# Performance work log

Hardware: AMD Instinct MI355X
Metric: run time of the kernel (lower is better)

The kernel has to match this reference:

```python
import jax, jax.numpy as jnp
import numpy as np
import math

L, H, E, D = 4, 8, 256, 32  # layers, heads, embed, head_dim
SCALE = 1.0 / math.sqrt(D)

def _ln(x, w, b, eps=1e-5):
    mu = jnp.mean(x, -1, keepdims=True)
    var = jnp.mean((x - mu) ** 2, -1, keepdims=True)
    return (x - mu) * jax.lax.rsqrt(var + eps) * w + b

def setup_inputs() -> dict:
    key = jax.random.key(0)
    ks = jax.random.split(key, 16)
    B, S, C = 32, 512, 512
    w = lambda k, sh: jax.random.normal(k, sh, jnp.float32) * 0.05
    return {
        'cnn_features': jax.random.normal(ks[0], (B, S, C), jnp.float32),
        'cnn_w': w(ks[1], (E, C)), 'cnn_b': jnp.zeros((E,), jnp.float32),
        'tok_emb': w(ks[2], (2, E)),
        'Wq': w(ks[3], (L, E, E)), 'bq': jnp.zeros((L, E), jnp.float32),
        'Wk': w(ks[4], (L, E, E)), 'bk': jnp.zeros((L, E), jnp.float32),
        'Wv': w(ks[5], (L, E, E)), 'bv': jnp.zeros((L, E), jnp.float32),
        'Wo': w(ks[6], (L, E, E)), 'bo': jnp.zeros((L, E), jnp.float32),
        'ln1_w': jnp.ones((L, E), jnp.float32), 'ln1_b': jnp.zeros((L, E), jnp.float32),
        'ln2_w': jnp.ones((L, E), jnp.float32), 'ln2_b': jnp.zeros((L, E), jnp.float32),
        'mlp_w1': w(ks[7], (L, 3 * E, E)), 'mlp_b1': jnp.zeros((L, 3 * E), jnp.float32),
        'mlp_w2': w(ks[8], (L, E, 3 * E)), 'mlp_b2': jnp.zeros((L, E), jnp.float32),
        'lnf_w': jnp.ones((E,), jnp.float32), 'lnf_b': jnp.zeros((E,), jnp.float32),
        'out_w1': w(ks[9], (2 * E, E)), 'out_b1': jnp.zeros((2 * E,), jnp.float32),
        'out_w2': w(ks[10], (C, 2 * E)), 'out_b2': jnp.zeros((C,), jnp.float32),
    }

def _forward(cnn_features, cnn_w, cnn_b, tok_emb, Wq, bq, Wk, bk, Wv, bv, Wo, bo,
             ln1_w, ln1_b, ln2_w, ln2_b, mlp_w1, mlp_b1, mlp_w2, mlp_b2,
             lnf_w, lnf_b, out_w1, out_b1, out_w2, out_b2):
    B, S, _ = cnn_features.shape
    # CNN feature projection + token-type embedding (all tokens type 0)
    x = cnn_features @ cnn_w.T + cnn_b + tok_emb[0]  # [B,S,E]
    for i in range(L):
        q = (x @ Wq[i].T + bq[i]).reshape(B, S, H, D).transpose(0, 2, 1, 3)
        k = (x @ Wk[i].T + bk[i]).reshape(B, S, H, D).transpose(0, 2, 1, 3)
        v = (x @ Wv[i].T + bv[i]).reshape(B, S, H, D).transpose(0, 2, 1, 3)
        scores = jnp.einsum('bhqd,bhkd->bhqk', q, k) * SCALE
        attn = jax.nn.softmax(scores, axis=-1)  # dropout = identity (eval)
        attended = jnp.einsum('bhqk,bhkd->bhqd', attn, v)
        attended = attended.transpose(0, 2, 1, 3).reshape(B, S, E)
        attn_out = attended @ Wo[i].T + bo[i]
        x = _ln(x + attn_out, ln1_w[i], ln1_b[i])
        h = jax.nn.gelu(x @ mlp_w1[i].T + mlp_b1[i], approximate=False)
        mlp_out = h @ mlp_w2[i].T + mlp_b2[i]
        x = _ln(x + mlp_out, ln2_w[i], ln2_b[i])
    x = _ln(x, lnf_w, lnf_b)
    h = jax.nn.gelu(x @ out_w1.T + out_b1, approximate=False)
    out = jax.nn.relu(h @ out_w2.T + out_b2)  # [B,S,cnn_feature_dim]
    return out

def reference(cnn_features, cnn_w, cnn_b, tok_emb, Wq, bq, Wk, bk, Wv, bv, Wo, bo,
              ln1_w, ln1_b, ln2_w, ln2_b, mlp_w1, mlp_b1, mlp_w2, mlp_b2,
              lnf_w, lnf_b, out_w1, out_b1, out_w2, out_b2):
    return _forward(cnn_features, cnn_w, cnn_b, tok_emb, Wq, bq, Wk, bk, Wv, bv, Wo, bo,
                    ln1_w, ln1_b, ln2_w, ln2_b, mlp_w1, mlp_b1, mlp_w2, mlp_b2,
                    lnf_w, lnf_b, out_w1, out_b1, out_w2, out_b2)
```

## Files before the change

kernel.cpp:

```cpp
#include <hip/hip_runtime.h>
#include <hip/hip_bf16.h>
#include <math.h>

#define B_SZ 32
#define S_SZ 512
#define C_SZ 512
#define E_SZ 256
#define H_SZ 8
#define D_SZ 32
#define L_SZ 4
#define N_TOK (B_SZ * S_SZ)
#define HID 768
#define MB (1048576)

typedef __attribute__((ext_vector_type(8))) short bf16x8;
typedef __attribute__((ext_vector_type(4))) float f32x4_t;

__device__ __forceinline__ float gelu_f(float x) {
    return 0.5f * x * (1.0f + erff(x * 0.70710678118654752f));
}

__device__ __forceinline__ ushort f2bf(float f) {
    uint u = __float_as_uint(f);
    return (ushort)((u + 0x7FFFu + ((u >> 16) & 1u)) >> 16);
}
__device__ __forceinline__ uint pack2(float a, float b) {
    __hip_bfloat162 h = __float22bfloat162_rn(make_float2(a, b));
    union { __hip_bfloat162 h; uint u; } c; c.h = h;
    return c.u;
}
__device__ __forceinline__ void unpack8(uint4 u, float* f) {
    f[0] = __uint_as_float((u.x & 0xFFFFu) << 16); f[1] = __uint_as_float(u.x & 0xFFFF0000u);
    f[2] = __uint_as_float((u.y & 0xFFFFu) << 16); f[3] = __uint_as_float(u.y & 0xFFFF0000u);
    f[4] = __uint_as_float((u.z & 0xFFFFu) << 16); f[5] = __uint_as_float(u.z & 0xFFFF0000u);
    f[6] = __uint_as_float((u.w & 0xFFFFu) << 16); f[7] = __uint_as_float(u.w & 0xFFFF0000u);
}

__device__ __forceinline__ void gload16(const ushort* g, ushort* l) {
    __builtin_amdgcn_global_load_lds(
        (const __attribute__((address_space(1))) void*)g,
        (__attribute__((address_space(3))) void*)l, 16, 0, 0);
}

__global__ __launch_bounds__(256)
void setup_kernel(const float* __restrict__ cnn, const float* __restrict__ cnn_w,
                  const float* __restrict__ Wo, const float* __restrict__ Wq,
                  const float* __restrict__ Wk, const float* __restrict__ Wv,
                  const float* __restrict__ mw1, const float* __restrict__ mw2,
                  const float* __restrict__ ow1, const float* __restrict__ ow2,
                  const float* __restrict__ bq, const float* __restrict__ bk,
                  const float* __restrict__ bv, ushort* __restrict__ cnnb,
                  ushort* __restrict__ wb, float* __restrict__ bqkv)
{
    const int bid = blockIdx.x, tid = threadIdx.x;
    if (bid < 4096) {
        const int i = (bid * 256 + tid) * 8;
        const float4 a = *(const float4*)(cnn + i);
        const float4 b = *(const float4*)(cnn + i + 4);
        uint4 o;
        o.x = pack2(a.x, a.y); o.y = pack2(a.z, a.w);
        o.z = pack2(b.x, b.y); o.w = pack2(b.z, b.w);
        *(uint4*)(cnnb + i) = o;
    } else if (bid < 5632) {
        const int i = ((bid - 4096) * 256 + tid) * 8;
        const float* src;
        if (i < 131072)       src = cnn_w + i;
        else if (i < 393216)  src = Wo + (i - 131072);
        else if (i < 1179648) {
            const int r = i - 393216;
            const int layer = r / 196608, rem = r % 196608;
            const int sub = rem >> 16, off = rem & 65535;
            src = (sub == 0 ? Wq : sub == 1 ? Wk : Wv) + layer * 65536 + off;
        }
        else if (i < 1966080) src = mw1 + (i - 1179648);
        else if (i < 2752512) src = mw2 + (i - 1966080);
        else if (i < 2883584) src = ow1 + (i - 2752512);
        else                  src = ow2 + (i - 2883584);
        const float4 a = *(const float4*)src;
        const float4 b = *(const float4*)(src + 4);
        uint4 o;
        o.x = pack2(a.x, a.y); o.y = pack2(a.z, a.w);
        o.z = pack2(b.x, b.y); o.w = pack2(b.z, b.w);
        *(uint4*)(wb + i) = o;
    } else {
        const int idx = (bid - 5632) * 256 + tid;
        const int layer = idx / 768, j = idx % 768;
        float v = (j < 256) ? bq[layer * 256 + j]
                : (j < 512) ? bk[layer * 256 + j - 256]
                            : bv[layer * 256 + j - 512];
        bqkv[layer * 768 + j] = v;
    }
}

template<int ACT, int EPI, bool OF, bool OB>
__global__ __launch_bounds__(256)
void gemm128_kernel(const ushort* __restrict__ A, const ushort* __restrict__ W,
                    const float* __restrict__ bias, const float* __restrict__ bias2,
                    float* __restrict__ Cf, ushort* __restrict__ Cb,
                    ushort* __restrict__ Cb2, int M, int K, int F)
{
    __shared__ __align__(16) ushort SMEM[32768];
    ushort* As0 = SMEM;
    ushort* Bs0 = SMEM + 16384;
    const int tid = threadIdx.x;
    const int bm = blockIdx.x * 128, bn = blockIdx.y * 128;
    const int lane = tid & 63, w = tid >> 6;
    const int lr8 = lane >> 3, lseg = lane & 7;
    const int lsx = lseg ^ lr8;
    const int wm = w >> 1, wn = w & 1;
    const int fr = lane & 15, fk = lane >> 4;
    const int fx = fr & 7;
    f32x4_t acc[4][4] = {};

    const ushort* Ag = A + (size_t)(bm + w * 32 + lr8) * K + lsx * 8;
    const ushort* Wg = W + (size_t)(bn + w * 32 + lr8) * K + lsx * 8;

    #pragma unroll
    for (int q = 0; q < 4; ++q) {
        gload16(Ag + (size_t)q * 8 * K, &As0[(w * 32 + q * 8) * 64]);
        gload16(Wg + (size_t)q * 8 * K, &Bs0[(w * 32 + q * 8) * 64]);
    }
    __syncthreads();

    const int NT = K >> 6;
    int cur = 0;
    for (int t = 0; t < NT; ++t) {
        if (t + 1 < NT) {
            const size_t k0 = (size_t)(t + 1) << 6;
            const int nb = (cur ^ 1) * 8192;
            #pragma unroll
            for (int q = 0; q < 4; ++q) {
                gload16(Ag + (size_t)q * 8 * K + k0, &As0[nb + (w * 32 + q * 8) * 64]);
                gload16(Wg + (size_t)q * 8 * K + k0, &Bs0[nb + (w * 32 + q * 8) * 64]);
            }
        }
        const int cb = cur * 8192;
        #pragma unroll
        for (int kk = 0; kk < 2; ++kk) {
            const int rs = ((kk * 4 + fk) ^ fx) * 8;
            bf16x8 af[4], bw[4];
            #pragma unroll
            for (int i = 0; i < 4; ++i)
                af[i] = *(const bf16x8*)&As0[cb + (wm * 64 + i * 16 + fr) * 64 + rs];
            #pragma unroll
            for (int j = 0; j < 4; ++j)
                bw[j] = *(const bf16x8*)&Bs0[cb + (wn * 64 + j * 16 + fr) * 64 + rs];
            #pragma unroll
            for (int i = 0; i < 4; ++i)
                #pragma unroll
                for (int j = 0; j < 4; ++j)
                    acc[i][j] = __builtin_amdgcn_mfma_f32_16x16x32_bf16(af[i], bw[j], acc[i][j], 0, 0, 0);
        }
        __syncthreads();
        cur ^= 1;
    }

    if (EPI == 1) {
        const bool vblk = (bn >= 512);
        #pragma unroll
        for (int j = 0; j < 4; ++j) {
            const int col = wn * 64 + j * 16 + fr;
            const float bb = bias[bn + col];
            #pragma unroll
            for (int i = 0; i < 4; ++i)
                #pragma unroll
                for (int r = 0; r < 4; ++r) {
                    const int row = wm * 64 + i * 16 + fk * 4 + r;
                    const ushort v = f2bf(acc[i][j][r] + bb);
                    if (vblk) SMEM[col * 136 + row] = v;
                    else      SMEM[row * 136 + col] = v;
                }
        }
        __syncthreads();
        if (vblk) {
            const int b2 = bm >> 9, r0 = bm & 511;
            #pragma unroll
            for (int it = 0; it < 8; ++it) {
                const int idx = tid + it * 256;
                const int d = idx >> 4, sc = idx & 15;
                const uint4 v = *(const uint4*)&SMEM[d * 136 + sc * 8];
                const int dd = bn - 512 + d;
                *(uint4*)&Cb2[((size_t)((b2 << 3) + (dd >> 5)) << 14)
                              + ((dd & 31) << 9) + r0 + sc * 8] = v;
            }
        } else {
            #pragma unroll
            for (int it = 0; it < 8; ++it) {
                const int idx = tid + it * 256;
                const int row = idx >> 4, ch = idx & 15;
                const uint4 v = *(const uint4*)&SMEM[row * 136 + ch * 8];
                *(uint4*)&Cb[(size_t)(bm + row) * 512 + bn + ch * 8] = v;
            }
        }
    } else {
        #pragma unroll
        for (int j = 0; j < 4; ++j) {
            const int col = bn + wn * 64 + j * 16 + fr;
            float bb = bias[col];
            if (bias2) bb += bias2[col];
            #pragma unroll
            for (int i = 0; i < 4; ++i)
                #pragma unroll
                for (int r = 0; r < 4; ++r) {
                    const int row = bm + wm * 64 + i * 16 + fk * 4 + r;
                    float t = acc[i][j][r] + bb;
                    if (ACT == 1) t = gelu_f(t);
                    if (ACT == 2) t = fmaxf(t, 0.0f);
                    if (OF) Cf[(size_t)row * F + col] = t;
                    if (OB) SMEM[(row - bm) * 136 + (col - bn)] = f2bf(t);
                }
        }
        if (OB) {
            __syncthreads();
            #pragma unroll
            for (int it = 0; it < 8; ++it) {
                const int idx = tid + it * 256;
                const int row = idx >> 4, ch = idx & 15;
                const uint4 v = *(const uint4*)&SMEM[row * 136 + ch * 8];
                *(uint4*)&Cb[(size_t)(bm + row) * F + bn + ch * 8] = v;
            }
        }
    }
}

template<bool FINAL>
__global__ __launch_bounds__(512)
void gemm_ln_kernel(const ushort* __restrict__ A, const ushort* __restrict__ W,
                    const float* __restrict__ bias, float* __restrict__ x,
                    ushort* __restrict__ xb, const float* __restrict__ lnw,
                    const float* __restrict__ lnb, const float* __restrict__ lnfw,
                    const float* __restrict__ lnfb, int K)
{
    __shared__ __align__(16) ushort As[2][64 * 64];
    __shared__ __align__(16) ushort Bs[2][256 * 64];
    __shared__ float psum[64][8], psq[64][8], murs[64][2];
    const int tid = threadIdx.x;
    const int bm = blockIdx.x * 64;
    const int lane = tid & 63, w = tid >> 6;
    const int lr8 = lane >> 3, lseg = lane & 7;
    const int lsx = lseg ^ lr8;
    const int fr = lane & 15, fk = lane >> 4;
    const int fx = fr & 7;
    f32x4_t acc[4][2] = {};

    const ushort* Ag = A + (size_t)(bm + w * 8 + lr8) * K + lsx * 8;
    const ushort* Wg = W + (size_t)(w * 32 + lr8) * K + lsx * 8;

    gload16(Ag, &As[0][(w * 8) * 64]);
    #pragma unroll
    for (int q = 0; q < 4; ++q) gload16(Wg + (size_t)q * 8 * K, &Bs[0][(w * 32 + q * 8) * 64]);
    __syncthreads();

    const int NT = K >> 6;
    int cur = 0;
    for (int t = 0; t < NT; ++t) {
        if (t + 1 < NT) {
            const size_t k0 = (size_t)(t + 1) << 6;
            gload16(Ag + k0, &As[cur ^ 1][(w * 8) * 64]);
            #pragma unroll
            for (int q = 0; q < 4; ++q)
                gload16(Wg + (size_t)q * 8 * K + k0, &Bs[cur ^ 1][(w * 32 + q * 8) * 64]);
        }
        bf16x8 af[2][4], bw[2][2];
        #pragma unroll
        for (int kk = 0; kk < 2; ++kk) {
            const int rs = ((kk * 4 + fk) ^ fx) * 8;
            #pragma unroll
            for (int i = 0; i < 4; ++i)
                af[kk][i] = *(const bf16x8*)&As[cur][(i * 16 + fr) * 64 + rs];
            #pragma unroll
            for (int j = 0; j < 2; ++j)
                bw[kk][j] = *(const bf16x8*)&Bs[cur][(w * 32 + j * 16 + fr) * 64 + rs];
        }
        #pragma unroll
        for (int kk = 0; kk < 2; ++kk)
            #pragma unroll
            for (int i = 0; i < 4; ++i)
                #pragma unroll
                for (int j = 0; j < 2; ++j)
                    acc[i][j] = __builtin_amdgcn_mfma_f32_16x16x32_bf16(af[kk][i], bw[kk][j], acc[i][j], 0, 0, 0);
        __syncthreads();
        cur ^= 1;
    }

    float y[4][2][4];
    #pragma unroll
    for (int j = 0; j < 2; ++j) {
        const int col = w * 32 + j * 16 + fr;
        const float bb = bias[col];
        #pragma unroll
        for (int i = 0; i < 4; ++i)
            #pragma unroll
            for (int r = 0; r < 4; ++r) {
                const int row = i * 16 + fk * 4 + r;
                y[i][j][r] = acc[i][j][r] + bb + x[(size_t)(bm + row) * 256 + col];
            }
    }
    #pragma unroll
    for (int i = 0; i < 4; ++i)
        #pragma unroll
        for (int r = 0; r < 4; ++r) {
            float s = y[i][0][r] + y[i][1][r];
            float q = y[i][0][r] * y[i][0][r] + y[i][1][r] * y[i][1][r];
            #pragma unroll
            for (int off = 1; off < 16; off <<= 1) {
                s += __shfl_xor(s, off);
                q += __shfl_xor(q, off);
            }
            if (fr == 0) {
                psum[i * 16 + fk * 4 + r][w] = s;
                psq [i * 16 + fk * 4 + r][w] = q;
            }
        }
    __syncthreads();
    if (tid < 64) {
        float ms = 0.f, mq = 0.f;
        #pragma unroll
        for (int ww = 0; ww < 8; ++ww) { ms += psum[tid][ww]; mq += psq[tid][ww]; }
        const float mu = ms * (1.0f / 256.0f);
        const float var = mq * (1.0f / 256.0f) - mu * mu;
        murs[tid][0] = mu;
        murs[tid][1] = rsqrtf(var + 1e-5f);
    }
    __syncthreads();
    #pragma unroll
    for (int i = 0; i < 4; ++i)
        #pragma unroll
        for (int r = 0; r < 4; ++r) {
            const int row = i * 16 + fk * 4 + r;
            const float mu = murs[row][0], rs = murs[row][1];
            #pragma unroll
            for (int j = 0; j < 2; ++j) {
                const int col = w * 32 + j * 16 + fr;
                const float xn = (y[i][j][r] - mu) * rs * lnw[col] + lnb[col];
                y[i][j][r] = xn;
                if (!FINAL) {
                    x [(size_t)(bm + row) * 256 + col] = xn;
                    xb[(size_t)(bm + row) * 256 + col] = f2bf(xn);
                }
            }
        }
    if (FINAL) {
        #pragma unroll
        for (int i = 0; i < 4; ++i)
            #pragma unroll
            for (int r = 0; r < 4; ++r) {
                float s = y[i][0][r] + y[i][1][r];
                float q = y[i][0][r] * y[i][0][r] + y[i][1][r] * y[i][1][r];
                #pragma unroll
                for (int off = 1; off < 16; off <<= 1) {
                    s += __shfl_xor(s, off);
                    q += __shfl_xor(q, off);
                }
                if (fr == 0) {
                    psum[i * 16 + fk * 4 + r][w] = s;
                    psq [i * 16 + fk * 4 + r][w] = q;
                }
            }
        __syncthreads();
        if (tid < 64) {
            float ms = 0.f, mq = 0.f;
            #pragma unroll
            for (int ww = 0; ww < 8; ++ww) { ms += psum[tid][ww]; mq += psq[tid][ww]; }
            const float mu = ms * (1.0f / 256.0f);
            const float var = mq * (1.0f / 256.0f) - mu * mu;
            murs[tid][0] = mu;
            murs[tid][1] = rsqrtf(var + 1e-5f);
        }
        __syncthreads();
        #pragma unroll
        for (int i = 0; i < 4; ++i)
            #pragma unroll
            for (int r = 0; r < 4; ++r) {
                const int row = i * 16 + fk * 4 + r;
                const float mu = murs[row][0], rs = murs[row][1];
                #pragma unroll
                for (int j = 0; j < 2; ++j) {
                    const int col = w * 32 + j * 16 + fr;
                    const float xn = (y[i][j][r] - mu) * rs * lnfw[col] + lnfb[col];
                    xb[(size_t)(bm + row) * 256 + col] = f2bf(xn);
                }
            }
    }
}

__global__ __launch_bounds__(512)
void attn_v5(const ushort* __restrict__ qk, const ushort* __restrict__ vt,
             ushort* __restrict__ out)
{
    __shared__ __align__(16) ushort Ks[512 * 40];
    __shared__ __align__(16) ushort Vs[32 * 520];
    const int bh = blockIdx.x, qc = blockIdx.y;
    const int b = bh >> 3, h = bh & 7;
    const int tid = threadIdx.x;
    const int w = tid >> 6, lane = tid & 63;
    const int g = lane >> 4, c = lane & 15;

    #pragma unroll
    for (int i = 0; i < 4; ++i) {
        const int idx = tid + i * 512;
        const int kr = idx >> 2, seg = idx & 3;
        const uint4 kv = *(const uint4*)(qk + ((size_t)b * 512 + kr) * 512
                                         + 256 + h * 32 + seg * 8);
        const int p = (((kr >> 2) & 1) << 4) | (((kr >> 3) & 3) << 2) | (kr & 3);
        const int pos = (kr & ~31) | p;
        *(uint4*)&Ks[pos * 40 + seg * 8] = kv;
        const int dr = idx >> 6, vseg = idx & 63;
        const uint4 vv = *(const uint4*)(vt + (size_t)bh * 16384 + dr * 512 + vseg * 8);
        *(uint4*)&Vs[dr * 520 + vseg * 8] = vv;
    }

    bf16x8 qf[2];
    #pragma unroll
    for (int j = 0; j < 2; ++j) {
        const size_t qrow = (size_t)b * 512 + qc * 256 + (j * 8 + w) * 16 + c;
        const uint4 qv = *(const uint4*)(qk + qrow * 512 + h * 32 + g * 8);
        float f[8]; unpack8(qv, f);
        const float scale = 0.25506806865756986f;
        union { uint u[4]; bf16x8 v; } qq;
        #pragma unroll
        for (int t = 0; t < 4; ++t) qq.u[t] = pack2(f[2*t] * scale, f[2*t+1] * scale);
        qf[j] = qq.v;
    }
    __syncthreads();

    const f32x4_t zz = {0.f, 0.f, 0.f, 0.f};
    #pragma unroll
    for (int j = 0; j < 2; ++j) {
        float m = -INFINITY, l = 0.f;
        f32x4_t o0 = zz, o1 = zz;
        for (int kt = 0; kt < 4; ++kt) {
            const int kbase = kt * 128;
            f32x4_t s[8];
            __builtin_amdgcn_s_setprio(1);
            #pragma unroll
            for (int kf = 0; kf < 8; ++kf) {
                const bf16x8 kfrag = *(const bf16x8*)&Ks[(kbase + kf * 16 + c) * 40 + g * 8];
                s[kf] = __builtin_amdgcn_mfma_f32_16x16x32_bf16(kfrag, qf[j], zz, 0, 0, 0);
            }
            __builtin_amdgcn_s_setprio(0);

            float mt = s[0][0];
            #pragma unroll
            for (int kf = 0; kf < 8; ++kf)
                #pragma unroll
                for (int r = 0; r < 4; ++r) mt = fmaxf(mt, s[kf][r]);
            mt = fmaxf(mt, __shfl_xor(mt, 16));
            mt = fmaxf(mt, __shfl_xor(mt, 32));
            const float mn = fmaxf(m, mt);
            const float corr = exp2f(m - mn);
            m = mn;
            float lt = 0.f;
            #pragma unroll
            for (int kf = 0; kf < 8; ++kf)
                #pragma unroll
                for (int r = 0; r < 4; ++r) {
                    const float p = exp2f(s[kf][r] - mn);
                    s[kf][r] = p; lt += p;
                }
            lt += __shfl_xor(lt, 16);
            lt += __shfl_xor(lt, 32);
            l = l * corr + lt;
            #pragma unroll
            for (int r = 0; r < 4; ++r) { o0[r] *= corr; o1[r] *= corr; }

            #pragma unroll
            for (int t = 0; t < 4; ++t) {
                union { uint u[4]; bf16x8 v; } pf;
                pf.u[0] = pack2(s[2*t][0],   s[2*t][1]);
                pf.u[1] = pack2(s[2*t][2],   s[2*t][3]);
                pf.u[2] = pack2(s[2*t+1][0], s[2*t+1][1]);
                pf.u[3] = pack2(s[2*t+1][2], s[2*t+1][3]);
                const bf16x8 va0 = *(const bf16x8*)&Vs[c * 520 + kbase + t * 32 + g * 8];
                const bf16x8 va1 = *(const bf16x8*)&Vs[(16 + c) * 520 + kbase + t * 32 + g * 8];
                __builtin_amdgcn_s_setprio(1);
                o0 = __builtin_amdgcn_mfma_f32_16x16x32_bf16(va0, pf.v, o0, 0, 0, 0);
                o1 = __builtin_amdgcn_mfma_f32_16x16x32_bf16(va1, pf.v, o1, 0, 0, 0);
                __builtin_amdgcn_s_setprio(0);
            }
        }

        const float inv = 1.0f / l;
        const size_t obase = ((size_t)b * 512 + qc * 256 + (j * 8 + w) * 16 + c) * 256 + h * 32;
        ushort4 w0, w1;
        w0.x = f2bf(o0[0] * inv); w0.y = f2bf(o0[1] * inv);
        w0.z = f2bf(o0[2] * inv); w0.w = f2bf(o0[3] * inv);
        w1.x = f2bf(o1[0] * inv); w1.y = f2bf(o1[1] * inv);
        w1.z = f2bf(o1[2] * inv); w1.w = f2bf(o1[3] * inv);
        *(ushort4*)(out + obase + g * 4)      = w0;
        *(ushort4*)(out + obase + 16 + g * 4) = w1;
    }
}

extern "C" void kernel_launch(void* const* d_in, const int* in_sizes, int n_in,
                              void* d_out, int out_size, void* d_ws, size_t ws_size,
                              hipStream_t stream)
{
    const float* cnn   = (const float*)d_in[0];
    const float* cnn_w = (const float*)d_in[1];
    const float* cnn_b = (const float*)d_in[2];
    const float* tok   = (const float*)d_in[3];
    const float* Wq    = (const float*)d_in[4];
    const float* bq    = (const float*)d_in[5];
    const float* Wk    = (const float*)d_in[6];
    const float* bk    = (const float*)d_in[7];
    const float* Wv    = (const float*)d_in[8];
    const float* bv    = (const float*)d_in[9];
    const float* Wo    = (const float*)d_in[10];
    const float* bo    = (const float*)d_in[11];
    const float* ln1w  = (const float*)d_in[12];
    const float* ln1b  = (const float*)d_in[13];
    const float* ln2w  = (const float*)d_in[14];
    const float* ln2b  = (const float*)d_in[15];
    const float* mw1   = (const float*)d_in[16];
    const float* mb1   = (const float*)d_in[17];
    const float* mw2   = (const float*)d_in[18];
    const float* mb2   = (const float*)d_in[19];
    const float* lnfw  = (const float*)d_in[20];
    const float* lnfb  = (const float*)d_in[21];
    const float* ow1   = (const float*)d_in[22];
    const float* ob1   = (const float*)d_in[23];
    const float* ow2   = (const float*)d_in[24];
    const float* ob2   = (const float*)d_in[25];

    const int M = N_TOK;
    char* ws = (char*)d_ws;

    float*  x     = (float*)(ws + 0);
    ushort* xb    = (ushort*)(ws + 16 * MB);
    ushort* qkb   = (ushort*)(ws + 24 * MB);
    ushort* cnnb  = (ushort*)(ws + 24 * MB);
    ushort* vt    = (ushort*)(ws + 40 * MB);
    ushort* ab_   = (ushort*)(ws + 48 * MB);
    ushort* hb_   = (ushort*)(ws + 40 * MB);
    ushort* wb    = (ushort*)(ws + 64 * MB);

    ushort* cnn_wb = wb;
    ushort* Wob    = wb + 131072;
    ushort* wqkv   = wb + 393216;
    ushort* mw1b   = wb + 1179648;
    ushort* mw2b   = wb + 1966080;
    ushort* ow1b   = wb + 2752512;
    ushort* ow2b   = wb + 2883584;
    float*  bqkv   = (float*)(ws + 64 * MB + 6291456);

    setup_kernel<<<dim3(5644), dim3(256), 0, stream>>>(
        cnn, cnn_w, Wo, Wq, Wk, Wv, mw1, mw2, ow1, ow2, bq, bk, bv,
        cnnb, wb, bqkv);

    gemm128_kernel<0, 0, true, true><<<dim3(M / 128, E_SZ / 128), dim3(256), 0, stream>>>(
        cnnb, cnn_wb, cnn_b, tok, x, xb, nullptr, M, C_SZ, E_SZ);

    for (int i = 0; i < L_SZ; ++i) {
        gemm128_kernel<0, 1, false, false><<<dim3(M / 128, HID / 128), dim3(256), 0, stream>>>(
            xb, wqkv + (size_t)i * 196608, bqkv + (size_t)i * 768, nullptr,
            nullptr, qkb, vt, M, E_SZ, HID);

        attn_v5<<<dim3(B_SZ * H_SZ, 2), dim3(512), 0, stream>>>(qkb, vt, ab_);

        gemm_ln_kernel<false><<<dim3(M / 64), dim3(512), 0, stream>>>(
            ab_, Wob + (size_t)i * 65536, bo + (size_t)i * E_SZ,
            x, xb, ln1w + (size_t)i * E_SZ, ln1b + (size_t)i * E_SZ,
            nullptr, nullptr, E_SZ);

        gemm128_kernel<1, 0, false, true><<<dim3(M / 128, HID / 128), dim3(256), 0, stream>>>(
            xb, mw1b + (size_t)i * HID * E_SZ, mb1 + (size_t)i * HID, nullptr,
            nullptr, hb_, nullptr, M, E_SZ, HID);

        if (i < L_SZ - 1) {
            gemm_ln_kernel<false><<<dim3(M / 64), dim3(512), 0, stream>>>(
                hb_, mw2b + (size_t)i * E_SZ * HID, mb2 + (size_t)i * E_SZ,
                x, xb, ln2w + (size_t)i * E_SZ, ln2b + (size_t)i * E_SZ,
                nullptr, nullptr, HID);
        } else {
            gemm_ln_kernel<true><<<dim3(M / 64), dim3(512), 0, stream>>>(
                hb_, mw2b + (size_t)i * E_SZ * HID, mb2 + (size_t)i * E_SZ,
                x, xb, ln2w + (size_t)i * E_SZ, ln2b + (size_t)i * E_SZ,
                lnfw, lnfb, HID);
        }
    }

    gemm128_kernel<1, 0, false, true><<<dim3(M / 128, (2 * E_SZ) / 128), dim3(256), 0, stream>>>(
        xb, ow1b, ob1, nullptr, nullptr, hb_, nullptr, M, E_SZ, 2 * E_SZ);
    gemm128_kernel<2, 0, true, false><<<dim3(M / 128, C_SZ / 128), dim3(256), 0, stream>>>(
        hb_, ow2b, ob2, nullptr, (float*)d_out, nullptr, nullptr, M, 2 * E_SZ, C_SZ);
}
```

Measured before the change: 548.4 us.

## Shrink GEMM N-tile to 64, use split waitcnt barriers, revert attention to one block per head

The generic GEMM tile goes from 128x128 to 128x64, doubling the grid and halving per-wave accumulators and LDS. The GEMM and GEMM+LN kernels now wait with explicit vmcnt counts and raw s_barrier so the next tile's loads can stay in flight across the barrier. Attention goes back to one block per (batch, head) covering all 512 queries instead of two query-half blocks. Smaller tiles add occupancy but reduce operand reuse, and the attention change halves the grid, so the net effect is unclear.

```diff
diff --git a/kernel.cpp b/kernel.cpp
--- a/kernel.cpp
+++ b/kernel.cpp
@@ -94,72 +94,77 @@
 
 template<int ACT, int EPI, bool OF, bool OB>
 __global__ __launch_bounds__(256)
-void gemm128_kernel(const ushort* __restrict__ A, const ushort* __restrict__ W,
-                    const float* __restrict__ bias, const float* __restrict__ bias2,
-                    float* __restrict__ Cf, ushort* __restrict__ Cb,
-                    ushort* __restrict__ Cb2, int M, int K, int F)
+void gemm_bt2_kernel(const ushort* __restrict__ A, const ushort* __restrict__ W,
+                     const float* __restrict__ bias, const float* __restrict__ bias2,
+                     float* __restrict__ Cf, ushort* __restrict__ Cb,
+                     ushort* __restrict__ Cb2, int M, int K, int F)
 {
-    __shared__ __align__(16) ushort SMEM[32768];
-    ushort* As0 = SMEM;
-    ushort* Bs0 = SMEM + 16384;
+    __shared__ __align__(16) ushort As[2][128 * 64];
+    __shared__ __align__(16) ushort Bs[2][64 * 64];
+    ushort* BOUNCE = &As[0][0];
     const int tid = threadIdx.x;
-    const int bm = blockIdx.x * 128, bn = blockIdx.y * 128;
+    const int bm = blockIdx.x * 128, bn = blockIdx.y * 64;
     const int lane = tid & 63, w = tid >> 6;
     const int lr8 = lane >> 3, lseg = lane & 7;
     const int lsx = lseg ^ lr8;
     const int wm = w >> 1, wn = w & 1;
     const int fr = lane & 15, fk = lane >> 4;
     const int fx = fr & 7;
-    f32x4_t acc[4][4] = {};
+    f32x4_t acc[4][2] = {};
 
     const ushort* Ag = A + (size_t)(bm + w * 32 + lr8) * K + lsx * 8;
-    const ushort* Wg = W + (size_t)(bn + w * 32 + lr8) * K + lsx * 8;
-
-    #pragma unroll
-    for (int q = 0; q < 4; ++q) {
-        gload16(Ag + (size_t)q * 8 * K, &As0[(w * 32 + q * 8) * 64]);
-        gload16(Wg + (size_t)q * 8 * K, &Bs0[(w * 32 + q * 8) * 64]);
-    }
-    __syncthreads();
+    const ushort* Wg = W + (size_t)(bn + w * 16 + lr8) * K + lsx * 8;
+
+    #pragma unroll
+    for (int q = 0; q < 4; ++q) gload16(Ag + (size_t)q * 8 * K, &As[0][(w * 32 + q * 8) * 64]);
+    #pragma unroll
+    for (int q = 0; q < 2; ++q) gload16(Wg + (size_t)q * 8 * K, &Bs[0][(w * 16 + q * 8) * 64]);
 
     const int NT = K >> 6;
     int cur = 0;
     for (int t = 0; t < NT; ++t) {
         if (t + 1 < NT) {
             const size_t k0 = (size_t)(t + 1) << 6;
-            const int nb = (cur ^ 1) * 8192;
-            #pragma unroll
-            for (int q = 0; q < 4; ++q) {
-                gload16(Ag + (size_t)q * 8 * K + k0, &As0[nb + (w * 32 + q * 8) * 64]);
-                gload16(Wg + (size_t)q * 8 * K + k0, &Bs0[nb + (w * 32 + q * 8) * 64]);
-            }
-        }
-        const int cb = cur * 8192;
+            #pragma unroll
+            for (int q = 0; q < 4; ++q)
+                gload16(Ag + (size_t)q * 8 * K + k0, &As[cur ^ 1][(w * 32 + q * 8) * 64]);
+            #pragma unroll
+            for (int q = 0; q < 2; ++q)
+                gload16(Wg + (size_t)q * 8 * K + k0, &Bs[cur ^ 1][(w * 16 + q * 8) * 64]);
+            asm volatile("s_waitcnt vmcnt(6)" ::: "memory");
+        } else {
+            asm volatile("s_waitcnt vmcnt(0)" ::: "memory");
+        }
+        __builtin_amdgcn_s_barrier();
+        asm volatile("" ::: "memory");
+        bf16x8 af[2][4], bw[2][2];
         #pragma unroll
         for (int kk = 0; kk < 2; ++kk) {
             const int rs = ((kk * 4 + fk) ^ fx) * 8;
-            bf16x8 af[4], bw[4];
             #pragma unroll
             for (int i = 0; i < 4; ++i)
-                af[i] = *(const bf16x8*)&As0[cb + (wm * 64 + i * 16 + fr) * 64 + rs];
-            #pragma unroll
-            for (int j = 0; j < 4; ++j)
-                bw[j] = *(const bf16x8*)&Bs0[cb + (wn * 64 + j * 16 + fr) * 64 + rs];
+                af[kk][i] = *(const bf16x8*)&As[cur][(wm * 64 + i * 16 + fr) * 64 + rs];
+            #pragma unroll
+            for (int j = 0; j < 2; ++j)
+                bw[kk][j] = *(const bf16x8*)&Bs[cur][(wn * 32 + j * 16 + fr) * 64 + rs];
+        }
+        #pragma unroll
+        for (int kk = 0; kk < 2; ++kk)
             #pragma unroll
             for (int i = 0; i < 4; ++i)
                 #pragma unroll
-                for (int j = 0; j < 4; ++j)
-                    acc[i][j] = __builtin_amdgcn_mfma_f32_16x16x32_bf16(af[i], bw[j], acc[i][j], 0, 0, 0);
-        }
-        __syncthreads();
+                for (int j = 0; j < 2; ++j)
+                    acc[i][j] = __builtin_amdgcn_mfma_f32_16x16x32_bf16(af[kk][i], bw[kk][j], acc[i][j], 0, 0, 0);
+        asm volatile("" ::: "memory");
+        __builtin_amdgcn_s_barrier();
         cur ^= 1;
     }
 
     if (EPI == 1) {
         const bool vblk = (bn >= 512);
         #pragma unroll
-        for (int j = 0; j < 4; ++j) {
-            const int col = wn * 64 + j * 16 + fr;
+        for (int j = 0; j < 2; ++j) {
+            const int col = wn * 32 + j * 16 + fr;
             const float bb = bias[bn + col];
             #pragma unroll
             for (int i = 0; i < 4; ++i)
@@ -167,35 +172,35 @@
                 for (int r = 0; r < 4; ++r) {
                     const int row = wm * 64 + i * 16 + fk * 4 + r;
                     const ushort v = f2bf(acc[i][j][r] + bb);
-                    if (vblk) SMEM[col * 136 + row] = v;
-                    else      SMEM[row * 136 + col] = v;
+                    if (vblk) BOUNCE[col * 136 + row] = v;
+                    else      BOUNCE[row * 72 + col] = v;
                 }
         }
         __syncthreads();
         if (vblk) {
             const int b2 = bm >> 9, r0 = bm & 511;
             #pragma unroll
-            for (int it = 0; it < 8; ++it) {
+            for (int it = 0; it < 4; ++it) {
                 const int idx = tid + it * 256;
                 const int d = idx >> 4, sc = idx & 15;
-                const uint4 v = *(const uint4*)&SMEM[d * 136 + sc * 8];
+                const uint4 v = *(const uint4*)&BOUNCE[d * 136 + sc * 8];
                 const int dd = bn - 512 + d;
                 *(uint4*)&Cb2[((size_t)((b2 << 3) + (dd >> 5)) << 14)
                               + ((dd & 31) << 9) + r0 + sc * 8] = v;
             }
         } else {
             #pragma unroll
-            for (int it = 0; it < 8; ++it) {
+            for (int it = 0; it < 4; ++it) {
                 const int idx = tid + it * 256;
-                const int row = idx >> 4, ch = idx & 15;
-                const uint4 v = *(const uint4*)&SMEM[row * 136 + ch * 8];
+                const int row = idx >> 3, ch = idx & 7;
+                const uint4 v = *(const uint4*)&BOUNCE[row * 72 + ch * 8];
                 *(uint4*)&Cb[(size_t)(bm + row) * 512 + bn + ch * 8] = v;
             }
         }
     } else {
         #pragma unroll
-        for (int j = 0; j < 4; ++j) {
-            const int col = bn + wn * 64 + j * 16 + fr;
+        for (int j = 0; j < 2; ++j) {
+            const int col = bn + wn * 32 + j * 16 + fr;
             float bb = bias[col];
             if (bias2) bb += bias2[col];
             #pragma unroll
@@ -207,16 +212,16 @@
                     if (ACT == 1) t = gelu_f(t);
                     if (ACT == 2) t = fmaxf(t, 0.0f);
                     if (OF) Cf[(size_t)row * F + col] = t;
-                    if (OB) SMEM[(row - bm) * 136 + (col - bn)] = f2bf(t);
+                    if (OB) BOUNCE[(row - bm) * 72 + (col - bn)] = f2bf(t);
                 }
         }
         if (OB) {
             __syncthreads();
             #pragma unroll
-            for (int it = 0; it < 8; ++it) {
+            for (int it = 0; it < 4; ++it) {
                 const int idx = tid + it * 256;
-                const int row = idx >> 4, ch = idx & 15;
-                const uint4 v = *(const uint4*)&SMEM[row * 136 + ch * 8];
+                const int row = idx >> 3, ch = idx & 7;
+                const uint4 v = *(const uint4*)&BOUNCE[row * 72 + ch * 8];
                 *(uint4*)&Cb[(size_t)(bm + row) * F + bn + ch * 8] = v;
             }
         }
@@ -249,7 +254,6 @@
     gload16(Ag, &As[0][(w * 8) * 64]);
     #pragma unroll
     for (int q = 0; q < 4; ++q) gload16(Wg + (size_t)q * 8 * K, &Bs[0][(w * 32 + q * 8) * 64]);
-    __syncthreads();
 
     const int NT = K >> 6;
     int cur = 0;
@@ -260,7 +264,12 @@
             #pragma unroll
             for (int q = 0; q < 4; ++q)
                 gload16(Wg + (size_t)q * 8 * K + k0, &Bs[cur ^ 1][(w * 32 + q * 8) * 64]);
-        }
+            asm volatile("s_waitcnt vmcnt(5)" ::: "memory");
+        } else {
+            asm volatile("s_waitcnt vmcnt(0)" ::: "memory");
+        }
+        __builtin_amdgcn_s_barrier();
+        asm volatile("" ::: "memory");
         bf16x8 af[2][4], bw[2][2];
         #pragma unroll
         for (int kk = 0; kk < 2; ++kk) {
@@ -279,7 +288,8 @@
                 #pragma unroll
                 for (int j = 0; j < 2; ++j)
                     acc[i][j] = __builtin_amdgcn_mfma_f32_16x16x32_bf16(af[kk][i], bw[kk][j], acc[i][j], 0, 0, 0);
-        __syncthreads();
+        asm volatile("" ::: "memory");
+        __builtin_amdgcn_s_barrier();
         cur ^= 1;
     }
 
@@ -341,6 +351,7 @@
             }
         }
     if (FINAL) {
+        __syncthreads();
         #pragma unroll
         for (int i = 0; i < 4; ++i)
             #pragma unroll
@@ -385,12 +396,12 @@
 }
 
 __global__ __launch_bounds__(512)
-void attn_v5(const ushort* __restrict__ qk, const ushort* __restrict__ vt,
+void attn_v4(const ushort* __restrict__ qk, const ushort* __restrict__ vt,
              ushort* __restrict__ out)
 {
     __shared__ __align__(16) ushort Ks[512 * 40];
     __shared__ __align__(16) ushort Vs[32 * 520];
-    const int bh = blockIdx.x, qc = blockIdx.y;
+    const int bh = blockIdx.x;
     const int b = bh >> 3, h = bh & 7;
     const int tid = threadIdx.x;
     const int w = tid >> 6, lane = tid & 63;
@@ -410,10 +421,10 @@
         *(uint4*)&Vs[dr * 520 + vseg * 8] = vv;
     }
 
-    bf16x8 qf[2];
-    #pragma unroll
-    for (int j = 0; j < 2; ++j) {
-        const size_t qrow = (size_t)b * 512 + qc * 256 + (j * 8 + w) * 16 + c;
+    bf16x8 qf[4];
+    #pragma unroll
+    for (int j = 0; j < 4; ++j) {
+        const size_t qrow = (size_t)b * 512 + (j * 8 + w) * 16 + c;
         const uint4 qv = *(const uint4*)(qk + qrow * 512 + h * 32 + g * 8);
         float f[8]; unpack8(qv, f);
         const float scale = 0.25506806865756986f;
@@ -426,7 +437,7 @@
 
     const f32x4_t zz = {0.f, 0.f, 0.f, 0.f};
     #pragma unroll
-    for (int j = 0; j < 2; ++j) {
+    for (int j = 0; j < 4; ++j) {
         float m = -INFINITY, l = 0.f;
         f32x4_t o0 = zz, o1 = zz;
         for (int kt = 0; kt < 4; ++kt) {
@@ -481,7 +492,7 @@
         }
 
         const float inv = 1.0f / l;
-        const size_t obase = ((size_t)b * 512 + qc * 256 + (j * 8 + w) * 16 + c) * 256 + h * 32;
+        const size_t obase = ((size_t)b * 512 + (j * 8 + w) * 16 + c) * 256 + h * 32;
         ushort4 w0, w1;
         w0.x = f2bf(o0[0] * inv); w0.y = f2bf(o0[1] * inv);
         w0.z = f2bf(o0[2] * inv); w0.w = f2bf(o0[3] * inv);
@@ -548,22 +559,22 @@
         cnn, cnn_w, Wo, Wq, Wk, Wv, mw1, mw2, ow1, ow2, bq, bk, bv,
         cnnb, wb, bqkv);
 
-    gemm128_kernel<0, 0, true, true><<<dim3(M / 128, E_SZ / 128), dim3(256), 0, stream>>>(
+    gemm_bt2_kernel<0, 0, true, true><<<dim3(M / 128, E_SZ / 64), dim3(256), 0, stream>>>(
         cnnb, cnn_wb, cnn_b, tok, x, xb, nullptr, M, C_SZ, E_SZ);
 
     for (int i = 0; i < L_SZ; ++i) {
-        gemm128_kernel<0, 1, false, false><<<dim3(M / 128, HID / 128), dim3(256), 0, stream>>>(
+        gemm_bt2_kernel<0, 1, false, false><<<dim3(M / 128, HID / 64), dim3(256), 0, stream>>>(
             xb, wqkv + (size_t)i * 196608, bqkv + (size_t)i * 768, nullptr,
             nullptr, qkb, vt, M, E_SZ, HID);
 
-        attn_v5<<<dim3(B_SZ * H_SZ, 2), dim3(512), 0, stream>>>(qkb, vt, ab_);
+        attn_v4<<<dim3(B_SZ * H_SZ), dim3(512), 0, stream>>>(qkb, vt, ab_);
 
         gemm_ln_kernel<false><<<dim3(M / 64), dim3(512), 0, stream>>>(
             ab_, Wob + (size_t)i * 65536, bo + (size_t)i * E_SZ,
             x, xb, ln1w + (size_t)i * E_SZ, ln1b + (size_t)i * E_SZ,
             nullptr, nullptr, E_SZ);
 
-        gemm128_kernel<1, 0, false, true><<<dim3(M / 128, HID / 128), dim3(256), 0, stream>>>(
+        gemm_bt2_kernel<1, 0, false, true><<<dim3(M / 128, HID / 64), dim3(256), 0, stream>>>(
             xb, mw1b + (size_t)i * HID * E_SZ, mb1 + (size_t)i * HID, nullptr,
             nullptr, hb_, nullptr, M, E_SZ, HID);
 
@@ -580,8 +591,8 @@
         }
     }
 
-    gemm128_kernel<1, 0, false, true><<<dim3(M / 128, (2 * E_SZ) / 128), dim3(256), 0, stream>>>(
+    gemm_bt2_kernel<1, 0, false, true><<<dim3(M / 128, (2 * E_SZ) / 64), dim3(256), 0, stream>>>(
         xb, ow1b, ob1, nullptr, nullptr, hb_, nullptr, M, E_SZ, 2 * E_SZ);
-    gemm128_kernel<2, 0, true, false><<<dim3(M / 128, C_SZ / 128), dim3(256), 0, stream>>>(
+    gemm_bt2_kernel<2, 0, true, false><<<dim3(M / 128, C_SZ / 64), dim3(256), 0, stream>>>(
         hb_, ow2b, ob2, nullptr, (float*)d_out, nullptr, nullptr, M, 2 * E_SZ, C_SZ);
 }
```

After: 510.9 us. 1.07x faster.
